# Optimization experiments

Hardware: AMD Instinct MI355X
Metric: run time of the kernel (lower is better)

## Reference

```python
import jax, jax.numpy as jnp
import numpy as np

IN_CAPS, IN_SIZE = 1152, 8
OUT_CAPS, OUT_SIZE = 10, 16
NUM_ITERS = 3


def squash(s, axis=-1, eps=1e-8):
    sq = jnp.sum(s * s, axis=axis, keepdims=True)
    norm = jnp.sqrt(sq + eps)
    return (sq / (1.0 + sq)) * (s / norm)


def setup_inputs() -> dict:
    key = jax.random.key(0)
    kx, kw = jax.random.split(key)
    x = jax.random.normal(kx, (512, IN_CAPS, IN_SIZE), dtype=jnp.float32)
    W = jax.random.normal(kw, (IN_CAPS, OUT_CAPS, OUT_SIZE, IN_SIZE), dtype=jnp.float32)
    return {"x": x, "W": W}


def reference(x, W):
    # u_hat[b,i,o,p] = sum_q W[i,o,p,q] x[b,i,q]   -> [B, I, O, P]
    u_hat = jnp.einsum("iopq,biq->biop", W, x)
    b_ij = jnp.zeros((IN_CAPS, OUT_CAPS), dtype=u_hat.dtype)
    v_j = None
    for _ in range(NUM_ITERS):
        # legacy F.softmax on [1,I,O,1] with no dim -> softmax over dim=1 (in_capsules)
        c_ij = jax.nn.softmax(b_ij, axis=0)                      # [I, O]
        s_j = jnp.einsum("io,biop->bop", c_ij, u_hat)            # [B, O, P]
        v_j = squash(s_j, axis=-1)                               # [B, O, P]
        # agreement, averaged over batch
        u_vj1 = jnp.einsum("biop,bop->io", u_hat, v_j) / x.shape[0]
        b_ij = b_ij + u_vj1
    return v_j  # [B, 10, 16]
```

## Files before the change

### kernel.cpp

```cpp
#include <hip/hip_runtime.h>
#include <hip/hip_bf16.h>

#define B 512
#define IC 1152
#define QD 8
#define OD 10
#define PD 16
#define KD (IC * QD)
#define NKB (KD / 32)
#define NCS 72
#define KSTEPS (NKB / NCS)
#define NCB 4
#define SOP (B * OD * PD)
#define IO (IC * OD)

typedef short bf16x8 __attribute__((ext_vector_type(8)));
typedef float f32x4 __attribute__((ext_vector_type(4)));

__device__ __forceinline__ short f2bf(float f) {
  union { float f; unsigned u; } x;
  x.f = f;
  unsigned r = x.u + 0x7FFFu + ((x.u >> 16) & 1u);
  return (short)(r >> 16);
}

__global__ __launch_bounds__(256) void routebuild_kernel(const float* __restrict__ W,
                                                         const float* __restrict__ u_part,
                                                         float* __restrict__ bijA,
                                                         short* __restrict__ Bs,
                                                         int mode) {
  __shared__ float bl[IO];
  __shared__ float wred[4][OD];
  __shared__ float mx[OD], inv[OD];
  const int tid = threadIdx.x;
  const int wave = tid >> 6, lane = tid & 63;

  if (mode != 0) {
    float lmax[OD];
#pragma unroll
    for (int o = 0; o < OD; ++o) lmax[o] = -1e30f;
    for (int i = tid; i < IC; i += 256) {
      float acc[OD];
      if (mode == 2) {
#pragma unroll
        for (int o = 0; o < OD; ++o) acc[o] = bijA[i * OD + o];
      } else {
#pragma unroll
        for (int o = 0; o < OD; ++o) acc[o] = 0.f;
      }
      for (int bc = 0; bc < NCB; ++bc) {
        const float* up = u_part + (size_t)bc * IO + i * OD;
        const float4 u0 = *(const float4*)up;
        const float4 u1 = *(const float4*)(up + 4);
        const float2 u2 = *(const float2*)(up + 8);
        acc[0] += u0.x; acc[1] += u0.y; acc[2] += u0.z; acc[3] += u0.w;
        acc[4] += u1.x; acc[5] += u1.y; acc[6] += u1.z; acc[7] += u1.w;
        acc[8] += u2.x; acc[9] += u2.y;
      }
#pragma unroll
      for (int o = 0; o < OD; ++o) {
        bl[i * OD + o] = acc[o];
        lmax[o] = fmaxf(lmax[o], acc[o]);
        if (mode == 1 && blockIdx.x == 0) bijA[i * OD + o] = acc[o];
      }
    }
#pragma unroll
    for (int o = 0; o < OD; ++o) {
      float m = lmax[o];
#pragma unroll
      for (int s = 1; s < 64; s <<= 1) m = fmaxf(m, __shfl_xor(m, s));
      if (lane == 0) wred[wave][o] = m;
    }
    __syncthreads();
    if (tid < OD)
      mx[tid] = fmaxf(fmaxf(wred[0][tid], wred[1][tid]),
                      fmaxf(wred[2][tid], wred[3][tid]));
    __syncthreads();
    float lsum[OD];
#pragma unroll
    for (int o = 0; o < OD; ++o) lsum[o] = 0.f;
    for (int i = tid; i < IC; i += 256) {
#pragma unroll
      for (int o = 0; o < OD; ++o) {
        const float e = __expf(bl[i * OD + o] - mx[o]);
        bl[i * OD + o] = e;
        lsum[o] += e;
      }
    }
    __syncthreads();
#pragma unroll
    for (int o = 0; o < OD; ++o) {
      float s = lsum[o];
#pragma unroll
      for (int st = 1; st < 64; st <<= 1) s += __shfl_xor(s, st);
      if (lane == 0) wred[wave][o] = s;
    }
    __syncthreads();
    if (tid < OD)
      inv[tid] = 1.f / (wred[0][tid] + wred[1][tid] + wred[2][tid] + wred[3][tid]);
    __syncthreads();
  }

  const int t = blockIdx.x * 256 + tid;
  const int kb = t / 160, n = t % 160;
  const int o = n >> 4, p = n & 15;
  short ov[32];
#pragma unroll
  for (int quad = 0; quad < 4; ++quad) {
    const int i = kb * 4 + quad;
    const float ci = (mode == 0) ? (1.0f / (float)IC) : (bl[i * OD + o] * inv[o]);
    const float4* wp = (const float4*)(W + (((size_t)i * OD + o) * PD + p) * QD);
    const float4 w0 = wp[0], w1 = wp[1];
    ov[quad * 8 + 0] = f2bf(ci * w0.x); ov[quad * 8 + 1] = f2bf(ci * w0.y);
    ov[quad * 8 + 2] = f2bf(ci * w0.z); ov[quad * 8 + 3] = f2bf(ci * w0.w);
    ov[quad * 8 + 4] = f2bf(ci * w1.x); ov[quad * 8 + 5] = f2bf(ci * w1.y);
    ov[quad * 8 + 6] = f2bf(ci * w1.z); ov[quad * 8 + 7] = f2bf(ci * w1.w);
  }
  int4* dst = (int4*)(Bs + (size_t)t * 32);
  const int4* src = (const int4*)ov;
#pragma unroll
  for (int j = 0; j < 4; ++j) dst[j] = src[j];
}

__global__ __launch_bounds__(256) void sgemm_kernel(const float* __restrict__ x,
                                                    const short* __restrict__ Bs,
                                                    float* __restrict__ s_part) {
  const int tid = threadIdx.x;
  const int wave = tid >> 6, lane = tid & 63;
  const int ln = lane & 15, quad = lane >> 4;
  const int cz = blockIdx.x % NCS, mb = blockIdx.x / NCS;
  const int m0 = mb * 64 + wave * 16;
  f32x4 acc[10] = {};
  const float* arow = x + (size_t)(m0 + ln) * KD + quad * 8;
#pragma unroll
  for (int step = 0; step < KSTEPS; ++step) {
    const int kb = cz * KSTEPS + step;
    const float* ap = arow + kb * 32;
    const f32x4 a0 = *(const f32x4*)ap;
    const f32x4 a1 = *(const f32x4*)(ap + 4);
    bf16x8 af;
    af[0] = f2bf(a0[0]); af[1] = f2bf(a0[1]); af[2] = f2bf(a0[2]); af[3] = f2bf(a0[3]);
    af[4] = f2bf(a1[0]); af[5] = f2bf(a1[1]); af[6] = f2bf(a1[2]); af[7] = f2bf(a1[3]);
    const short* bp = Bs + (size_t)kb * 5120 + ln * 32 + quad * 8;
#pragma unroll
    for (int nt = 0; nt < 10; ++nt) {
      const bf16x8 bf = *(const bf16x8*)(bp + nt * 512);
      acc[nt] = __builtin_amdgcn_mfma_f32_16x16x32_bf16(af, bf, acc[nt], 0, 0, 0);
    }
  }
  float* sp = s_part + (size_t)cz * SOP;
#pragma unroll
  for (int nt = 0; nt < 10; ++nt)
#pragma unroll
    for (int r = 0; r < 4; ++r)
      sp[(size_t)(m0 + quad * 4 + r) * 160 + nt * 16 + ln] = acc[nt][r];
}

__global__ __launch_bounds__(256) void squash_kernel(const float* __restrict__ s_part,
                                                     short* __restrict__ vB,
                                                     float* __restrict__ out,
                                                     int write_out) {
  const int t = blockIdx.x * 256 + threadIdx.x;
  float sv = 0.f;
#pragma unroll 8
  for (int ch = 0; ch < NCS; ++ch) sv += s_part[(size_t)ch * SOP + t];
  float sq = sv * sv;
#pragma unroll
  for (int m = 1; m < 16; m <<= 1) sq += __shfl_xor(sq, m, 16);
  const float norm = sqrtf(sq + 1e-8f);
  const float val = sv * (sq / ((1.f + sq) * norm));
  if (write_out) {
    out[t] = val;
  } else {
    const int b = t / 160, n = t - b * 160;
    vB[((size_t)(b >> 5) * 160 + n) * 32 + (b & 31)] = f2bf(val);
  }
}

__global__ __launch_bounds__(256) void aggemm_kernel(const float* __restrict__ x,
                                                     const float* __restrict__ W,
                                                     const short* __restrict__ vB,
                                                     float* __restrict__ u_part) {
  __shared__ __align__(16) short Abuf[16 * 64 * 8];
  const int tid = threadIdx.x;
  const int ig8 = blockIdx.x, kq = blockIdx.y;
  const int b0 = kq * 128;
#pragma unroll
  for (int j = 0; j < 8; ++j) {
    const int idx = tid + j * 256;
    const int b = idx >> 4, f4 = idx & 15;
    const float4 vx = *(const float4*)(x + (size_t)(b0 + b) * KD + ig8 * 64 + f4 * 4);
    const int kb = b >> 5, qk = (b & 31) >> 3, jj = b & 7;
    const int mt = (f4 * 4) >> 4;
    const int mlb = (f4 & 3) * 4;
    short* dst = Abuf + (((mt * 4 + kb) * 64 + qk * 16 + mlb) * 8 + jj);
    dst[0] = f2bf(vx.x); dst[8] = f2bf(vx.y); dst[16] = f2bf(vx.z); dst[24] = f2bf(vx.w);
  }
  __syncthreads();
  const int mt = tid >> 6, lane = tid & 63;
  const int ln = lane & 15, quad = lane >> 4;
  f32x4 acc[10] = {};
#pragma unroll
  for (int kb = 0; kb < 4; ++kb) {
    const bf16x8 af = *(const bf16x8*)(Abuf + ((mt * 4 + kb) * 64 + lane) * 8);
    const short* bp = vB + ((size_t)(kq * 4 + kb) * 160 + ln) * 32 + quad * 8;
#pragma unroll
    for (int nt = 0; nt < 10; ++nt) {
      const bf16x8 bf = *(const bf16x8*)(bp + nt * 512);
      acc[nt] = __builtin_amdgcn_mfma_f32_16x16x32_bf16(af, bf, acc[nt], 0, 0, 0);
    }
  }
  const int i = ig8 * 8 + mt * 2 + (quad >> 1);
  const int qb = (quad & 1) * 4;
#pragma unroll
  for (int nt = 0; nt < 10; ++nt) {
    const float4 wv = *(const float4*)(W + (((size_t)i * OD + nt) * PD + ln) * QD + qb);
    float pa = acc[nt][0] * wv.x + acc[nt][1] * wv.y + acc[nt][2] * wv.z + acc[nt][3] * wv.w;
    pa += __shfl_xor(pa, 1); pa += __shfl_xor(pa, 2); pa += __shfl_xor(pa, 4);
    pa += __shfl_xor(pa, 8); pa += __shfl_xor(pa, 16);
    if ((lane & 31) == 0)
      u_part[(size_t)kq * IO + i * OD + nt] = pa * (1.0f / (float)B);
  }
}


extern "C" void kernel_launch(void* const* d_in, const int* in_sizes, int n_in,
                              void* d_out, int out_size, void* d_ws, size_t ws_size,
                              hipStream_t stream) {
  const float* x = (const float*)d_in[0];
  const float* W = (const float*)d_in[1];
  float* out = (float*)d_out;

  float* ws = (float*)d_ws;
  float* s_part = ws;
  float* bijA = s_part + (size_t)NCS * SOP;
  float* u_part = bijA + IO;
  short* vB = (short*)(u_part + (size_t)NCB * IO);
  short* Bs = vB + (size_t)16 * 160 * 32;

  const dim3 agrid(144, NCB);

  routebuild_kernel<<<180, 256, 0, stream>>>(W, u_part, bijA, Bs, 0);
  sgemm_kernel<<<8 * NCS, 256, 0, stream>>>(x, Bs, s_part);
  squash_kernel<<<SOP / 256, 256, 0, stream>>>(s_part, vB, out, 0);
  aggemm_kernel<<<agrid, 256, 0, stream>>>(x, W, vB, u_part);
  routebuild_kernel<<<180, 256, 0, stream>>>(W, u_part, bijA, Bs, 1);
  sgemm_kernel<<<8 * NCS, 256, 0, stream>>>(x, Bs, s_part);
  squash_kernel<<<SOP / 256, 256, 0, stream>>>(s_part, vB, out, 0);
  aggemm_kernel<<<agrid, 256, 0, stream>>>(x, W, vB, u_part);
  routebuild_kernel<<<180, 256, 0, stream>>>(W, u_part, bijA, Bs, 2);
  sgemm_kernel<<<8 * NCS, 256, 0, stream>>>(x, Bs, s_part);
  squash_kernel<<<SOP / 256, 256, 0, stream>>>(s_part, vB, out, 1);
}
```

Before: 184.4 us.

## Fuse routing softmax, s-GEMM and squash into one per-output-capsule kernel

Replaces the routebuild/sgemm/squash sequence with one iter_kernel per routing iteration. Each of 80 blocks owns one output capsule and 64 batch rows: it computes that capsule's softmax column and runs the full-K MFMA reduction, scaling W on the fly. It then squashes in registers and writes vB or the output. The agreement kernel now loops over all batch chunks inside one block, so u_t needs no cross-block partial sums and the split-K partial buffers go away. This cuts launches and large partial-sum traffic, but only 80 or 144 blocks run, each doing a long serial K loop, which may leave much of the GPU idle.

```diff
diff --git a/kernel.cpp b/kernel.cpp
--- a/kernel.cpp
+++ b/kernel.cpp
@@ -8,10 +8,6 @@
 #define PD 16
 #define KD (IC * QD)
 #define NKB (KD / 32)
-#define NCS 72
-#define KSTEPS (NKB / NCS)
-#define NCB 4
-#define SOP (B * OD * PD)
 #define IO (IC * OD)
 
 typedef short bf16x8 __attribute__((ext_vector_type(8)));
@@ -23,191 +19,148 @@
   unsigned r = x.u + 0x7FFFu + ((x.u >> 16) & 1u);
   return (short)(r >> 16);
 }
+__device__ __forceinline__ unsigned pkbf(float a, float b) {
+  union { __hip_bfloat162 h; unsigned u; } c;
+  c.h = __float22bfloat162_rn(make_float2(a, b));
+  return c.u;
+}
 
-__global__ __launch_bounds__(256) void routebuild_kernel(const float* __restrict__ W,
-                                                         const float* __restrict__ u_part,
-                                                         float* __restrict__ bijA,
-                                                         short* __restrict__ Bs,
-                                                         int mode) {
-  __shared__ float bl[IO];
-  __shared__ float wred[4][OD];
-  __shared__ float mx[OD], inv[OD];
+__global__ __launch_bounds__(256) void iter_kernel(const float* __restrict__ x,
+                                                   const float* __restrict__ W,
+                                                   const float* __restrict__ u_t,
+                                                   float* __restrict__ bijA,
+                                                   short* __restrict__ vB,
+                                                   float* __restrict__ out,
+                                                   int mode) {
+  __shared__ float cS[IC];
+  __shared__ float redA[4], redB[4];
   const int tid = threadIdx.x;
+  const int mb = blockIdx.x & 7, o = blockIdx.x >> 3;
   const int wave = tid >> 6, lane = tid & 63;
+  const int ln = lane & 15, quad = lane >> 4;
 
+  float inv = 0.f;
   if (mode != 0) {
-    float lmax[OD];
+    float lm = -1e30f;
 #pragma unroll
-    for (int o = 0; o < OD; ++o) lmax[o] = -1e30f;
-    for (int i = tid; i < IC; i += 256) {
-      float acc[OD];
-      if (mode == 2) {
-#pragma unroll
-        for (int o = 0; o < OD; ++o) acc[o] = bijA[i * OD + o];
-      } else {
-#pragma unroll
-        for (int o = 0; o < OD; ++o) acc[o] = 0.f;
-      }
-      for (int bc = 0; bc < NCB; ++bc) {
-        const float* up = u_part + (size_t)bc * IO + i * OD;
-        const float4 u0 = *(const float4*)up;
-        const float4 u1 = *(const float4*)(up + 4);
-        const float2 u2 = *(const float2*)(up + 8);
-        acc[0] += u0.x; acc[1] += u0.y; acc[2] += u0.z; acc[3] += u0.w;
-        acc[4] += u1.x; acc[5] += u1.y; acc[6] += u1.z; acc[7] += u1.w;
-        acc[8] += u2.x; acc[9] += u2.y;
-      }
-#pragma unroll
-      for (int o = 0; o < OD; ++o) {
-        bl[i * OD + o] = acc[o];
-        lmax[o] = fmaxf(lmax[o], acc[o]);
-        if (mode == 1 && blockIdx.x == 0) bijA[i * OD + o] = acc[o];
+    for (int k = 0; k < 5; ++k) {
+      const int i = tid + k * 256;
+      if (i < IC) {
+        float t = u_t[o * IC + i];
+        if (mode == 2) t += bijA[o * IC + i];
+        if (mode == 1 && mb == 0) bijA[o * IC + i] = t;
+        cS[i] = t;
+        lm = fmaxf(lm, t);
       }
     }
 #pragma unroll
-    for (int o = 0; o < OD; ++o) {
-      float m = lmax[o];
+    for (int s = 1; s < 64; s <<= 1) lm = fmaxf(lm, __shfl_xor(lm, s));
+    if (lane == 0) redA[wave] = lm;
+    __syncthreads();
+    const float mx = fmaxf(fmaxf(redA[0], redA[1]), fmaxf(redA[2], redA[3]));
+    float ls = 0.f;
 #pragma unroll
-      for (int s = 1; s < 64; s <<= 1) m = fmaxf(m, __shfl_xor(m, s));
-      if (lane == 0) wred[wave][o] = m;
+    for (int k = 0; k < 5; ++k) {
+      const int i = tid + k * 256;
+      if (i < IC) {
+        const float e = __expf(cS[i] - mx);
+        cS[i] = e;
+        ls += e;
+      }
     }
+#pragma unroll
+    for (int s = 1; s < 64; s <<= 1) ls += __shfl_xor(ls, s);
+    if (lane == 0) redB[wave] = ls;
     __syncthreads();
-    if (tid < OD)
-      mx[tid] = fmaxf(fmaxf(wred[0][tid], wred[1][tid]),
-                      fmaxf(wred[2][tid], wred[3][tid]));
+    inv = 1.f / (redB[0] + redB[1] + redB[2] + redB[3]);
+  }
+
+  const int m0 = mb * 64 + wave * 16;
+  const float* arow = x + (size_t)(m0 + ln) * KD + quad * 8;
+  const float* wrow = W + (o * PD + ln) * QD;
+  const float cu = 1.0f / (float)IC;
+  f32x4 acc0 = {}, acc1 = {};
+#pragma unroll 2
+  for (int kb = 0; kb < NKB; kb += 2) {
+    {
+      const int i = kb * 4 + quad;
+      const float ci = mode ? cS[i] * inv : cu;
+      const f32x4 a0 = *(const f32x4*)(arow + (size_t)kb * 32);
+      const f32x4 a1 = *(const f32x4*)(arow + (size_t)kb * 32 + 4);
+      const f32x4 w0 = *(const f32x4*)(wrow + (size_t)i * 1280);
+      const f32x4 w1 = *(const f32x4*)(wrow + (size_t)i * 1280 + 4);
+      uint4 ap, bp;
+      ap.x = pkbf(a0[0], a0[1]); ap.y = pkbf(a0[2], a0[3]);
+      ap.z = pkbf(a1[0], a1[1]); ap.w = pkbf(a1[2], a1[3]);
+      bp.x = pkbf(ci * w0[0], ci * w0[1]); bp.y = pkbf(ci * w0[2], ci * w0[3]);
+      bp.z = pkbf(ci * w1[0], ci * w1[1]); bp.w = pkbf(ci * w1[2], ci * w1[3]);
+      acc0 = __builtin_amdgcn_mfma_f32_16x16x32_bf16(*(bf16x8*)&ap, *(bf16x8*)&bp, acc0, 0, 0, 0);
+    }
+    {
+      const int i = (kb + 1) * 4 + quad;
+      const float ci = mode ? cS[i] * inv : cu;
+      const f32x4 a0 = *(const f32x4*)(arow + (size_t)(kb + 1) * 32);
+      const f32x4 a1 = *(const f32x4*)(arow + (size_t)(kb + 1) * 32 + 4);
+      const f32x4 w0 = *(const f32x4*)(wrow + (size_t)i * 1280);
+      const f32x4 w1 = *(const f32x4*)(wrow + (size_t)i * 1280 + 4);
+      uint4 ap, bp;
+      ap.x = pkbf(a0[0], a0[1]); ap.y = pkbf(a0[2], a0[3]);
+      ap.z = pkbf(a1[0], a1[1]); ap.w = pkbf(a1[2], a1[3]);
+      bp.x = pkbf(ci * w0[0], ci * w0[1]); bp.y = pkbf(ci * w0[2], ci * w0[3]);
+      bp.z = pkbf(ci * w1[0], ci * w1[1]); bp.w = pkbf(ci * w1[2], ci * w1[3]);
+      acc1 = __builtin_amdgcn_mfma_f32_16x16x32_bf16(*(bf16x8*)&ap, *(bf16x8*)&bp, acc1, 0, 0, 0);
+    }
+  }
+  const f32x4 acc = acc0 + acc1;
+#pragma unroll
+  for (int r = 0; r < 4; ++r) {
+    float sq = acc[r] * acc[r];
+    sq += __shfl_xor(sq, 1); sq += __shfl_xor(sq, 2);
+    sq += __shfl_xor(sq, 4); sq += __shfl_xor(sq, 8);
+    const float norm = sqrtf(sq + 1e-8f);
+    const float val = acc[r] * (sq / ((1.f + sq) * norm));
+    const int b = m0 + quad * 4 + r;
+    if (mode == 2) {
+      out[((size_t)b * OD + o) * PD + ln] = val;
+    } else {
+      vB[((size_t)(b >> 5) * 160 + o * PD + ln) * 32 + (b & 31)] = f2bf(val);
+    }
+  }
+}
+
+__global__ __launch_bounds__(256) void agg_kernel(const float* __restrict__ x,
+                                                  const float* __restrict__ W,
+                                                  const short* __restrict__ vB,
+                                                  float* __restrict__ u_t) {
+  __shared__ __align__(16) short Abuf[16 * 64 * 8];
+  const int tid = threadIdx.x;
+  const int ig8 = blockIdx.x;
+  const int mt = tid >> 6, lane = tid & 63;
+  const int ln = lane & 15, quad = lane >> 4;
+  f32x4 acc[10] = {};
+  for (int kq = 0; kq < 4; ++kq) {
+    const int b0 = kq * 128;
     __syncthreads();
-    float lsum[OD];
 #pragma unroll
-    for (int o = 0; o < OD; ++o) lsum[o] = 0.f;
-    for (int i = tid; i < IC; i += 256) {
-#pragma unroll
-      for (int o = 0; o < OD; ++o) {
-        const float e = __expf(bl[i * OD + o] - mx[o]);
-        bl[i * OD + o] = e;
-        lsum[o] += e;
-      }
+    for (int j = 0; j < 8; ++j) {
+      const int idx = tid + j * 256;
+      const int b = idx >> 4, f4 = idx & 15;
+      const float4 vx = *(const float4*)(x + (size_t)(b0 + b) * KD + ig8 * 64 + f4 * 4);
+      const int kbl = b >> 5, qk = (b & 31) >> 3, jj = b & 7;
+      const int mtt = f4 >> 2, mlb = (f4 & 3) * 4;
+      short* dst = Abuf + (((mtt * 4 + kbl) * 64 + qk * 16 + mlb) * 8 + jj);
+      dst[0] = f2bf(vx.x); dst[8] = f2bf(vx.y); dst[16] = f2bf(vx.z); dst[24] = f2bf(vx.w);
     }
     __syncthreads();
 #pragma unroll
-    for (int o = 0; o < OD; ++o) {
-      float s = lsum[o];
+    for (int kbb = 0; kbb < 4; ++kbb) {
+      const bf16x8 af = *(const bf16x8*)(Abuf + ((mt * 4 + kbb) * 64 + lane) * 8);
+      const short* bp = vB + ((size_t)((kq * 4 + kbb) * 160) + ln) * 32 + quad * 8;
 #pragma unroll
-      for (int st = 1; st < 64; st <<= 1) s += __shfl_xor(s, st);
-      if (lane == 0) wred[wave][o] = s;
-    }
-    __syncthreads();
-    if (tid < OD)
-      inv[tid] = 1.f / (wred[0][tid] + wred[1][tid] + wred[2][tid] + wred[3][tid]);
-    __syncthreads();
-  }
-
-  const int t = blockIdx.x * 256 + tid;
-  const int kb = t / 160, n = t % 160;
-  const int o = n >> 4, p = n & 15;
-  short ov[32];
-#pragma unroll
-  for (int quad = 0; quad < 4; ++quad) {
-    const int i = kb * 4 + quad;
-    const float ci = (mode == 0) ? (1.0f / (float)IC) : (bl[i * OD + o] * inv[o]);
-    const float4* wp = (const float4*)(W + (((size_t)i * OD + o) * PD + p) * QD);
-    const float4 w0 = wp[0], w1 = wp[1];
-    ov[quad * 8 + 0] = f2bf(ci * w0.x); ov[quad * 8 + 1] = f2bf(ci * w0.y);
-    ov[quad * 8 + 2] = f2bf(ci * w0.z); ov[quad * 8 + 3] = f2bf(ci * w0.w);
-    ov[quad * 8 + 4] = f2bf(ci * w1.x); ov[quad * 8 + 5] = f2bf(ci * w1.y);
-    ov[quad * 8 + 6] = f2bf(ci * w1.z); ov[quad * 8 + 7] = f2bf(ci * w1.w);
-  }
-  int4* dst = (int4*)(Bs + (size_t)t * 32);
-  const int4* src = (const int4*)ov;
-#pragma unroll
-  for (int j = 0; j < 4; ++j) dst[j] = src[j];
-}
-
-__global__ __launch_bounds__(256) void sgemm_kernel(const float* __restrict__ x,
-                                                    const short* __restrict__ Bs,
-                                                    float* __restrict__ s_part) {
-  const int tid = threadIdx.x;
-  const int wave = tid >> 6, lane = tid & 63;
-  const int ln = lane & 15, quad = lane >> 4;
-  const int cz = blockIdx.x % NCS, mb = blockIdx.x / NCS;
-  const int m0 = mb * 64 + wave * 16;
-  f32x4 acc[10] = {};
-  const float* arow = x + (size_t)(m0 + ln) * KD + quad * 8;
-#pragma unroll
-  for (int step = 0; step < KSTEPS; ++step) {
-    const int kb = cz * KSTEPS + step;
-    const float* ap = arow + kb * 32;
-    const f32x4 a0 = *(const f32x4*)ap;
-    const f32x4 a1 = *(const f32x4*)(ap + 4);
-    bf16x8 af;
-    af[0] = f2bf(a0[0]); af[1] = f2bf(a0[1]); af[2] = f2bf(a0[2]); af[3] = f2bf(a0[3]);
-    af[4] = f2bf(a1[0]); af[5] = f2bf(a1[1]); af[6] = f2bf(a1[2]); af[7] = f2bf(a1[3]);
-    const short* bp = Bs + (size_t)kb * 5120 + ln * 32 + quad * 8;
-#pragma unroll
-    for (int nt = 0; nt < 10; ++nt) {
-      const bf16x8 bf = *(const bf16x8*)(bp + nt * 512);
-      acc[nt] = __builtin_amdgcn_mfma_f32_16x16x32_bf16(af, bf, acc[nt], 0, 0, 0);
-    }
-  }
-  float* sp = s_part + (size_t)cz * SOP;
-#pragma unroll
-  for (int nt = 0; nt < 10; ++nt)
-#pragma unroll
-    for (int r = 0; r < 4; ++r)
-      sp[(size_t)(m0 + quad * 4 + r) * 160 + nt * 16 + ln] = acc[nt][r];
-}
-
-__global__ __launch_bounds__(256) void squash_kernel(const float* __restrict__ s_part,
-                                                     short* __restrict__ vB,
-                                                     float* __restrict__ out,
-                                                     int write_out) {
-  const int t = blockIdx.x * 256 + threadIdx.x;
-  float sv = 0.f;
-#pragma unroll 8
-  for (int ch = 0; ch < NCS; ++ch) sv += s_part[(size_t)ch * SOP + t];
-  float sq = sv * sv;
-#pragma unroll
-  for (int m = 1; m < 16; m <<= 1) sq += __shfl_xor(sq, m, 16);
-  const float norm = sqrtf(sq + 1e-8f);
-  const float val = sv * (sq / ((1.f + sq) * norm));
-  if (write_out) {
-    out[t] = val;
-  } else {
-    const int b = t / 160, n = t - b * 160;
-    vB[((size_t)(b >> 5) * 160 + n) * 32 + (b & 31)] = f2bf(val);
-  }
-}
-
-__global__ __launch_bounds__(256) void aggemm_kernel(const float* __restrict__ x,
-                                                     const float* __restrict__ W,
-                                                     const short* __restrict__ vB,
-                                                     float* __restrict__ u_part) {
-  __shared__ __align__(16) short Abuf[16 * 64 * 8];
-  const int tid = threadIdx.x;
-  const int ig8 = blockIdx.x, kq = blockIdx.y;
-  const int b0 = kq * 128;
-#pragma unroll
-  for (int j = 0; j < 8; ++j) {
-    const int idx = tid + j * 256;
-    const int b = idx >> 4, f4 = idx & 15;
-    const float4 vx = *(const float4*)(x + (size_t)(b0 + b) * KD + ig8 * 64 + f4 * 4);
-    const int kb = b >> 5, qk = (b & 31) >> 3, jj = b & 7;
-    const int mt = (f4 * 4) >> 4;
-    const int mlb = (f4 & 3) * 4;
-    short* dst = Abuf + (((mt * 4 + kb) * 64 + qk * 16 + mlb) * 8 + jj);
-    dst[0] = f2bf(vx.x); dst[8] = f2bf(vx.y); dst[16] = f2bf(vx.z); dst[24] = f2bf(vx.w);
-  }
-  __syncthreads();
-  const int mt = tid >> 6, lane = tid & 63;
-  const int ln = lane & 15, quad = lane >> 4;
-  f32x4 acc[10] = {};
-#pragma unroll
-  for (int kb = 0; kb < 4; ++kb) {
-    const bf16x8 af = *(const bf16x8*)(Abuf + ((mt * 4 + kb) * 64 + lane) * 8);
-    const short* bp = vB + ((size_t)(kq * 4 + kb) * 160 + ln) * 32 + quad * 8;
-#pragma unroll
-    for (int nt = 0; nt < 10; ++nt) {
-      const bf16x8 bf = *(const bf16x8*)(bp + nt * 512);
-      acc[nt] = __builtin_amdgcn_mfma_f32_16x16x32_bf16(af, bf, acc[nt], 0, 0, 0);
+      for (int nt = 0; nt < 10; ++nt) {
+        const bf16x8 bf = *(const bf16x8*)(bp + nt * 512);
+        acc[nt] = __builtin_amdgcn_mfma_f32_16x16x32_bf16(af, bf, acc[nt], 0, 0, 0);
+      }
     }
   }
   const int i = ig8 * 8 + mt * 2 + (quad >> 1);
@@ -218,8 +171,7 @@
     float pa = acc[nt][0] * wv.x + acc[nt][1] * wv.y + acc[nt][2] * wv.z + acc[nt][3] * wv.w;
     pa += __shfl_xor(pa, 1); pa += __shfl_xor(pa, 2); pa += __shfl_xor(pa, 4);
     pa += __shfl_xor(pa, 8); pa += __shfl_xor(pa, 16);
-    if ((lane & 31) == 0)
-      u_part[(size_t)kq * IO + i * OD + nt] = pa * (1.0f / (float)B);
+    if ((lane & 31) == 0) u_t[(size_t)nt * IC + i] = pa * (1.0f / (float)B);
   }
 }
 
@@ -232,23 +184,13 @@
   float* out = (float*)d_out;
 
   float* ws = (float*)d_ws;
-  float* s_part = ws;
-  float* bijA = s_part + (size_t)NCS * SOP;
-  float* u_part = bijA + IO;
-  short* vB = (short*)(u_part + (size_t)NCB * IO);
-  short* Bs = vB + (size_t)16 * 160 * 32;
+  float* u_t = ws;
+  float* bijA = u_t + IO;
+  short* vB = (short*)(bijA + IO);
 
-  const dim3 agrid(144, NCB);
-
-  routebuild_kernel<<<180, 256, 0, stream>>>(W, u_part, bijA, Bs, 0);
-  sgemm_kernel<<<8 * NCS, 256, 0, stream>>>(x, Bs, s_part);
-  squash_kernel<<<SOP / 256, 256, 0, stream>>>(s_part, vB, out, 0);
-  aggemm_kernel<<<agrid, 256, 0, stream>>>(x, W, vB, u_part);
-  routebuild_kernel<<<180, 256, 0, stream>>>(W, u_part, bijA, Bs, 1);
-  sgemm_kernel<<<8 * NCS, 256, 0, stream>>>(x, Bs, s_part);
-  squash_kernel<<<SOP / 256, 256, 0, stream>>>(s_part, vB, out, 0);
-  aggemm_kernel<<<agrid, 256, 0, stream>>>(x, W, vB, u_part);
-  routebuild_kernel<<<180, 256, 0, stream>>>(W, u_part, bijA, Bs, 2);
-  sgemm_kernel<<<8 * NCS, 256, 0, stream>>>(x, Bs, s_part);
-  squash_kernel<<<SOP / 256, 256, 0, stream>>>(s_part, vB, out, 1);
+  iter_kernel<<<80, 256, 0, stream>>>(x, W, u_t, bijA, vB, out, 0);
+  agg_kernel<<<144, 256, 0, stream>>>(x, W, vB, u_t);
+  iter_kernel<<<80, 256, 0, stream>>>(x, W, u_t, bijA, vB, out, 1);
+  agg_kernel<<<144, 256, 0, stream>>>(x, W, vB, u_t);
+  iter_kernel<<<80, 256, 0, stream>>>(x, W, u_t, bijA, vB, out, 2);
 }
```

Result: slower. 524.1 us (+184.3%).

## Fuse dependent stages into paired kernels synchronized by global atomic counters

Applied to the files above, without the earlier changes.

Merges each sgemm+squash pair and each agreement-GEMM+route-build pair into single launches. Consumer blocks spin on a device-scope atomic counter until all producer blocks finish, which cuts the number of kernel launches and the gaps between them. The agreement GEMM now loops over the four batch chunks inside each block, so the four-way u_part partial reduction is gone, and u is written transposed. The spin-wait depends on all producer blocks being resident or scheduled ahead of the waiting blocks, which risks deadlock or idle CUs while consumers spin.

```diff
diff --git a/kernel.cpp b/kernel.cpp
--- a/kernel.cpp
+++ b/kernel.cpp
@@ -10,9 +10,11 @@
 #define NKB (KD / 32)
 #define NCS 72
 #define KSTEPS (NKB / NCS)
-#define NCB 4
+#define SUNITS 576
+#define AUNITS 144
+#define RBBLK 180
+#define IO (IC * OD)
 #define SOP (B * OD * PD)
-#define IO (IC * OD)
 
 typedef short bf16x8 __attribute__((ext_vector_type(8)));
 typedef float f32x4 __attribute__((ext_vector_type(4)));
@@ -24,44 +26,177 @@
   return (short)(r >> 16);
 }
 
-__global__ __launch_bounds__(256) void routebuild_kernel(const float* __restrict__ W,
-                                                         const float* __restrict__ u_part,
-                                                         float* __restrict__ bijA,
-                                                         short* __restrict__ Bs,
-                                                         int mode) {
-  __shared__ float bl[IO];
-  __shared__ float wred[4][OD];
-  __shared__ float mx[OD], inv[OD];
+__device__ __forceinline__ void signal_done(int* cnt) {
+  __syncthreads();
+  if (threadIdx.x == 0) {
+    __threadfence();
+    __hip_atomic_fetch_add(cnt, 1, __ATOMIC_RELEASE, __HIP_MEMORY_SCOPE_AGENT);
+  }
+}
+__device__ __forceinline__ void wait_done(int* cnt, int target) {
+  if (threadIdx.x == 0) {
+    while (__hip_atomic_load(cnt, __ATOMIC_RELAXED, __HIP_MEMORY_SCOPE_AGENT) < target)
+      __builtin_amdgcn_s_sleep(8);
+    __threadfence();
+  }
+  __syncthreads();
+}
+
+__global__ __launch_bounds__(256) void rb0_kernel(const float* __restrict__ W,
+                                                  short* __restrict__ Bs,
+                                                  int* __restrict__ cnt) {
+  if (blockIdx.x == 0 && threadIdx.x < 8) cnt[threadIdx.x] = 0;
+  const int t = blockIdx.x * 256 + threadIdx.x;
+  const int kb = t / 160, n = t % 160;
+  const int o = n >> 4, p = n & 15;
+  const float cu = 1.0f / (float)IC;
+  short ov[32];
+#pragma unroll
+  for (int quad = 0; quad < 4; ++quad) {
+    const int i = kb * 4 + quad;
+    const float4* wp = (const float4*)(W + (((size_t)i * OD + o) * PD + p) * QD);
+    const float4 w0 = wp[0], w1 = wp[1];
+    ov[quad * 8 + 0] = f2bf(cu * w0.x); ov[quad * 8 + 1] = f2bf(cu * w0.y);
+    ov[quad * 8 + 2] = f2bf(cu * w0.z); ov[quad * 8 + 3] = f2bf(cu * w0.w);
+    ov[quad * 8 + 4] = f2bf(cu * w1.x); ov[quad * 8 + 5] = f2bf(cu * w1.y);
+    ov[quad * 8 + 6] = f2bf(cu * w1.z); ov[quad * 8 + 7] = f2bf(cu * w1.w);
+  }
+  int4* dst = (int4*)(Bs + (size_t)t * 32);
+  const int4* src = (const int4*)ov;
+#pragma unroll
+  for (int j = 0; j < 4; ++j) dst[j] = src[j];
+}
+
+__global__ __launch_bounds__(256) void d1_kernel(const float* __restrict__ x,
+                                                 const short* __restrict__ Bs,
+                                                 float* __restrict__ s_part,
+                                                 short* __restrict__ vB,
+                                                 float* __restrict__ out,
+                                                 int* __restrict__ cnt,
+                                                 int write_out) {
   const int tid = threadIdx.x;
-  const int wave = tid >> 6, lane = tid & 63;
-
-  if (mode != 0) {
+  if (blockIdx.x < SUNITS) {
+    const int wave = tid >> 6, lane = tid & 63;
+    const int ln = lane & 15, quad = lane >> 4;
+    const int cz = blockIdx.x % NCS, mb = blockIdx.x / NCS;
+    const int m0 = mb * 64 + wave * 16;
+    f32x4 acc[10] = {};
+    const float* arow = x + (size_t)(m0 + ln) * KD + quad * 8;
+#pragma unroll
+    for (int step = 0; step < KSTEPS; ++step) {
+      const int kb = cz * KSTEPS + step;
+      const float* ap = arow + (size_t)kb * 32;
+      const f32x4 a0 = *(const f32x4*)ap;
+      const f32x4 a1 = *(const f32x4*)(ap + 4);
+      bf16x8 af;
+      af[0] = f2bf(a0[0]); af[1] = f2bf(a0[1]); af[2] = f2bf(a0[2]); af[3] = f2bf(a0[3]);
+      af[4] = f2bf(a1[0]); af[5] = f2bf(a1[1]); af[6] = f2bf(a1[2]); af[7] = f2bf(a1[3]);
+      const short* bp = Bs + (size_t)kb * 5120 + ln * 32 + quad * 8;
+#pragma unroll
+      for (int nt = 0; nt < 10; ++nt) {
+        const bf16x8 bf = *(const bf16x8*)(bp + nt * 512);
+        acc[nt] = __builtin_amdgcn_mfma_f32_16x16x32_bf16(af, bf, acc[nt], 0, 0, 0);
+      }
+    }
+    float* sp = s_part + (size_t)cz * SOP;
+#pragma unroll
+    for (int nt = 0; nt < 10; ++nt)
+#pragma unroll
+      for (int r = 0; r < 4; ++r)
+        sp[(size_t)(m0 + quad * 4 + r) * 160 + nt * 16 + ln] = acc[nt][r];
+    signal_done(cnt);
+  } else {
+    wait_done(cnt, SUNITS);
+    const int t = (blockIdx.x - SUNITS) * 256 + tid;
+    float sv = 0.f;
+#pragma unroll 8
+    for (int ch = 0; ch < NCS; ++ch) sv += s_part[(size_t)ch * SOP + t];
+    float sq = sv * sv;
+#pragma unroll
+    for (int m = 1; m < 16; m <<= 1) sq += __shfl_xor(sq, m, 16);
+    const float norm = sqrtf(sq + 1e-8f);
+    const float val = sv * (sq / ((1.f + sq) * norm));
+    if (write_out) {
+      out[t] = val;
+    } else {
+      const int b = t / 160, n = t - b * 160;
+      vB[((size_t)(b >> 5) * 160 + n) * 32 + (b & 31)] = f2bf(val);
+    }
+  }
+}
+
+__global__ __launch_bounds__(256) void d2_kernel(const float* __restrict__ x,
+                                                 const float* __restrict__ W,
+                                                 const short* __restrict__ vB,
+                                                 float* __restrict__ u_t,
+                                                 float* __restrict__ bijA,
+                                                 short* __restrict__ Bs,
+                                                 int* __restrict__ cnt,
+                                                 int mode) {
+  __shared__ __align__(16) char smem[48000];
+  const int tid = threadIdx.x;
+  if (blockIdx.x < AUNITS) {
+    short* Abuf = (short*)smem;
+    const int ig8 = blockIdx.x;
+    const int mt = tid >> 6, lane = tid & 63;
+    const int ln = lane & 15, quad = lane >> 4;
+    f32x4 acc[10] = {};
+    for (int kq = 0; kq < 4; ++kq) {
+      const int b0 = kq * 128;
+      __syncthreads();
+#pragma unroll
+      for (int j = 0; j < 8; ++j) {
+        const int idx = tid + j * 256;
+        const int b = idx >> 4, f4 = idx & 15;
+        const float4 vx = *(const float4*)(x + (size_t)(b0 + b) * KD + ig8 * 64 + f4 * 4);
+        const int kbl = b >> 5, qk = (b & 31) >> 3, jj = b & 7;
+        const int mtt = f4 >> 2, mlb = (f4 & 3) * 4;
+        short* dst = Abuf + (((mtt * 4 + kbl) * 64 + qk * 16 + mlb) * 8 + jj);
+        dst[0] = f2bf(vx.x); dst[8] = f2bf(vx.y); dst[16] = f2bf(vx.z); dst[24] = f2bf(vx.w);
+      }
+      __syncthreads();
+#pragma unroll
+      for (int kbb = 0; kbb < 4; ++kbb) {
+        const bf16x8 af = *(const bf16x8*)(Abuf + ((mt * 4 + kbb) * 64 + lane) * 8);
+        const short* bp = vB + ((size_t)((kq * 4 + kbb) * 160) + ln) * 32 + quad * 8;
+#pragma unroll
+        for (int nt = 0; nt < 10; ++nt) {
+          const bf16x8 bf = *(const bf16x8*)(bp + nt * 512);
+          acc[nt] = __builtin_amdgcn_mfma_f32_16x16x32_bf16(af, bf, acc[nt], 0, 0, 0);
+        }
+      }
+    }
+    const int lane2 = tid & 63;
+    const int ln2 = lane2 & 15, quad2 = lane2 >> 4;
+    const int i = ig8 * 8 + (tid >> 6) * 2 + (quad2 >> 1);
+    const int qb = (quad2 & 1) * 4;
+#pragma unroll
+    for (int nt = 0; nt < 10; ++nt) {
+      const float4 wv = *(const float4*)(W + (((size_t)i * OD + nt) * PD + ln2) * QD + qb);
+      float pa = acc[nt][0] * wv.x + acc[nt][1] * wv.y + acc[nt][2] * wv.z + acc[nt][3] * wv.w;
+      pa += __shfl_xor(pa, 1); pa += __shfl_xor(pa, 2); pa += __shfl_xor(pa, 4);
+      pa += __shfl_xor(pa, 8); pa += __shfl_xor(pa, 16);
+      if ((lane2 & 31) == 0) u_t[(size_t)nt * IC + i] = pa * (1.0f / (float)B);
+    }
+    signal_done(cnt);
+  } else {
+    float* bl = (float*)smem;
+    __shared__ float wred[4][OD];
+    __shared__ float mxS[OD], invS[OD];
+    const int tb = blockIdx.x - AUNITS;
+    const int wave = tid >> 6, lane = tid & 63;
+    wait_done(cnt, AUNITS);
     float lmax[OD];
 #pragma unroll
     for (int o = 0; o < OD; ++o) lmax[o] = -1e30f;
     for (int i = tid; i < IC; i += 256) {
-      float acc[OD];
-      if (mode == 2) {
-#pragma unroll
-        for (int o = 0; o < OD; ++o) acc[o] = bijA[i * OD + o];
-      } else {
-#pragma unroll
-        for (int o = 0; o < OD; ++o) acc[o] = 0.f;
-      }
-      for (int bc = 0; bc < NCB; ++bc) {
-        const float* up = u_part + (size_t)bc * IO + i * OD;
-        const float4 u0 = *(const float4*)up;
-        const float4 u1 = *(const float4*)(up + 4);
-        const float2 u2 = *(const float2*)(up + 8);
-        acc[0] += u0.x; acc[1] += u0.y; acc[2] += u0.z; acc[3] += u0.w;
-        acc[4] += u1.x; acc[5] += u1.y; acc[6] += u1.z; acc[7] += u1.w;
-        acc[8] += u2.x; acc[9] += u2.y;
-      }
 #pragma unroll
       for (int o = 0; o < OD; ++o) {
-        bl[i * OD + o] = acc[o];
-        lmax[o] = fmaxf(lmax[o], acc[o]);
-        if (mode == 1 && blockIdx.x == 0) bijA[i * OD + o] = acc[o];
+        float t = u_t[o * IC + i];
+        if (mode == 2) t += bijA[o * IC + i];
+        if (mode == 1 && tb == 0) bijA[o * IC + i] = t;
+        bl[i * OD + o] = t;
+        lmax[o] = fmaxf(lmax[o], t);
       }
     }
 #pragma unroll
@@ -73,8 +208,8 @@
     }
     __syncthreads();
     if (tid < OD)
-      mx[tid] = fmaxf(fmaxf(wred[0][tid], wred[1][tid]),
-                      fmaxf(wred[2][tid], wred[3][tid]));
+      mxS[tid] = fmaxf(fmaxf(wred[0][tid], wred[1][tid]),
+                       fmaxf(wred[2][tid], wred[3][tid]));
     __syncthreads();
     float lsum[OD];
 #pragma unroll
@@ -82,7 +217,7 @@
     for (int i = tid; i < IC; i += 256) {
 #pragma unroll
       for (int o = 0; o < OD; ++o) {
-        const float e = __expf(bl[i * OD + o] - mx[o]);
+        const float e = __expf(bl[i * OD + o] - mxS[o]);
         bl[i * OD + o] = e;
         lsum[o] += e;
       }
@@ -97,129 +232,27 @@
     }
     __syncthreads();
     if (tid < OD)
-      inv[tid] = 1.f / (wred[0][tid] + wred[1][tid] + wred[2][tid] + wred[3][tid]);
-    __syncthreads();
-  }
-
-  const int t = blockIdx.x * 256 + tid;
-  const int kb = t / 160, n = t % 160;
-  const int o = n >> 4, p = n & 15;
-  short ov[32];
-#pragma unroll
-  for (int quad = 0; quad < 4; ++quad) {
-    const int i = kb * 4 + quad;
-    const float ci = (mode == 0) ? (1.0f / (float)IC) : (bl[i * OD + o] * inv[o]);
-    const float4* wp = (const float4*)(W + (((size_t)i * OD + o) * PD + p) * QD);
-    const float4 w0 = wp[0], w1 = wp[1];
-    ov[quad * 8 + 0] = f2bf(ci * w0.x); ov[quad * 8 + 1] = f2bf(ci * w0.y);
-    ov[quad * 8 + 2] = f2bf(ci * w0.z); ov[quad * 8 + 3] = f2bf(ci * w0.w);
-    ov[quad * 8 + 4] = f2bf(ci * w1.x); ov[quad * 8 + 5] = f2bf(ci * w1.y);
-    ov[quad * 8 + 6] = f2bf(ci * w1.z); ov[quad * 8 + 7] = f2bf(ci * w1.w);
-  }
-  int4* dst = (int4*)(Bs + (size_t)t * 32);
-  const int4* src = (const int4*)ov;
-#pragma unroll
-  for (int j = 0; j < 4; ++j) dst[j] = src[j];
-}
-
-__global__ __launch_bounds__(256) void sgemm_kernel(const float* __restrict__ x,
-                                                    const short* __restrict__ Bs,
-                                                    float* __restrict__ s_part) {
-  const int tid = threadIdx.x;
-  const int wave = tid >> 6, lane = tid & 63;
-  const int ln = lane & 15, quad = lane >> 4;
-  const int cz = blockIdx.x % NCS, mb = blockIdx.x / NCS;
-  const int m0 = mb * 64 + wave * 16;
-  f32x4 acc[10] = {};
-  const float* arow = x + (size_t)(m0 + ln) * KD + quad * 8;
-#pragma unroll
-  for (int step = 0; step < KSTEPS; ++step) {
-    const int kb = cz * KSTEPS + step;
-    const float* ap = arow + kb * 32;
-    const f32x4 a0 = *(const f32x4*)ap;
-    const f32x4 a1 = *(const f32x4*)(ap + 4);
-    bf16x8 af;
-    af[0] = f2bf(a0[0]); af[1] = f2bf(a0[1]); af[2] = f2bf(a0[2]); af[3] = f2bf(a0[3]);
-    af[4] = f2bf(a1[0]); af[5] = f2bf(a1[1]); af[6] = f2bf(a1[2]); af[7] = f2bf(a1[3]);
-    const short* bp = Bs + (size_t)kb * 5120 + ln * 32 + quad * 8;
-#pragma unroll
-    for (int nt = 0; nt < 10; ++nt) {
-      const bf16x8 bf = *(const bf16x8*)(bp + nt * 512);
-      acc[nt] = __builtin_amdgcn_mfma_f32_16x16x32_bf16(af, bf, acc[nt], 0, 0, 0);
-    }
-  }
-  float* sp = s_part + (size_t)cz * SOP;
-#pragma unroll
-  for (int nt = 0; nt < 10; ++nt)
-#pragma unroll
-    for (int r = 0; r < 4; ++r)
-      sp[(size_t)(m0 + quad * 4 + r) * 160 + nt * 16 + ln] = acc[nt][r];
-}
-
-__global__ __launch_bounds__(256) void squash_kernel(const float* __restrict__ s_part,
-                                                     short* __restrict__ vB,
-                                                     float* __restrict__ out,
-                                                     int write_out) {
-  const int t = blockIdx.x * 256 + threadIdx.x;
-  float sv = 0.f;
-#pragma unroll 8
-  for (int ch = 0; ch < NCS; ++ch) sv += s_part[(size_t)ch * SOP + t];
-  float sq = sv * sv;
-#pragma unroll
-  for (int m = 1; m < 16; m <<= 1) sq += __shfl_xor(sq, m, 16);
-  const float norm = sqrtf(sq + 1e-8f);
-  const float val = sv * (sq / ((1.f + sq) * norm));
-  if (write_out) {
-    out[t] = val;
-  } else {
-    const int b = t / 160, n = t - b * 160;
-    vB[((size_t)(b >> 5) * 160 + n) * 32 + (b & 31)] = f2bf(val);
-  }
-}
-
-__global__ __launch_bounds__(256) void aggemm_kernel(const float* __restrict__ x,
-                                                     const float* __restrict__ W,
-                                                     const short* __restrict__ vB,
-                                                     float* __restrict__ u_part) {
-  __shared__ __align__(16) short Abuf[16 * 64 * 8];
-  const int tid = threadIdx.x;
-  const int ig8 = blockIdx.x, kq = blockIdx.y;
-  const int b0 = kq * 128;
-#pragma unroll
-  for (int j = 0; j < 8; ++j) {
-    const int idx = tid + j * 256;
-    const int b = idx >> 4, f4 = idx & 15;
-    const float4 vx = *(const float4*)(x + (size_t)(b0 + b) * KD + ig8 * 64 + f4 * 4);
-    const int kb = b >> 5, qk = (b & 31) >> 3, jj = b & 7;
-    const int mt = (f4 * 4) >> 4;
-    const int mlb = (f4 & 3) * 4;
-    short* dst = Abuf + (((mt * 4 + kb) * 64 + qk * 16 + mlb) * 8 + jj);
-    dst[0] = f2bf(vx.x); dst[8] = f2bf(vx.y); dst[16] = f2bf(vx.z); dst[24] = f2bf(vx.w);
-  }
-  __syncthreads();
-  const int mt = tid >> 6, lane = tid & 63;
-  const int ln = lane & 15, quad = lane >> 4;
-  f32x4 acc[10] = {};
-#pragma unroll
-  for (int kb = 0; kb < 4; ++kb) {
-    const bf16x8 af = *(const bf16x8*)(Abuf + ((mt * 4 + kb) * 64 + lane) * 8);
-    const short* bp = vB + ((size_t)(kq * 4 + kb) * 160 + ln) * 32 + quad * 8;
-#pragma unroll
-    for (int nt = 0; nt < 10; ++nt) {
-      const bf16x8 bf = *(const bf16x8*)(bp + nt * 512);
-      acc[nt] = __builtin_amdgcn_mfma_f32_16x16x32_bf16(af, bf, acc[nt], 0, 0, 0);
-    }
-  }
-  const int i = ig8 * 8 + mt * 2 + (quad >> 1);
-  const int qb = (quad & 1) * 4;
-#pragma unroll
-  for (int nt = 0; nt < 10; ++nt) {
-    const float4 wv = *(const float4*)(W + (((size_t)i * OD + nt) * PD + ln) * QD + qb);
-    float pa = acc[nt][0] * wv.x + acc[nt][1] * wv.y + acc[nt][2] * wv.z + acc[nt][3] * wv.w;
-    pa += __shfl_xor(pa, 1); pa += __shfl_xor(pa, 2); pa += __shfl_xor(pa, 4);
-    pa += __shfl_xor(pa, 8); pa += __shfl_xor(pa, 16);
-    if ((lane & 31) == 0)
-      u_part[(size_t)kq * IO + i * OD + nt] = pa * (1.0f / (float)B);
+      invS[tid] = 1.f / (wred[0][tid] + wred[1][tid] + wred[2][tid] + wred[3][tid]);
+    __syncthreads();
+    const int t = tb * 256 + tid;
+    const int kb = t / 160, n = t % 160;
+    const int o = n >> 4, p = n & 15;
+    short ov[32];
+#pragma unroll
+    for (int quad = 0; quad < 4; ++quad) {
+      const int i = kb * 4 + quad;
+      const float ci = bl[i * OD + o] * invS[o];
+      const float4* wp = (const float4*)(W + (((size_t)i * OD + o) * PD + p) * QD);
+      const float4 w0 = wp[0], w1 = wp[1];
+      ov[quad * 8 + 0] = f2bf(ci * w0.x); ov[quad * 8 + 1] = f2bf(ci * w0.y);
+      ov[quad * 8 + 2] = f2bf(ci * w0.z); ov[quad * 8 + 3] = f2bf(ci * w0.w);
+      ov[quad * 8 + 4] = f2bf(ci * w1.x); ov[quad * 8 + 5] = f2bf(ci * w1.y);
+      ov[quad * 8 + 6] = f2bf(ci * w1.z); ov[quad * 8 + 7] = f2bf(ci * w1.w);
+    }
+    int4* dst = (int4*)(Bs + (size_t)t * 32);
+    const int4* src = (const int4*)ov;
+#pragma unroll
+    for (int j = 0; j < 4; ++j) dst[j] = src[j];
   }
 }
 
@@ -233,22 +266,16 @@
 
   float* ws = (float*)d_ws;
   float* s_part = ws;
-  float* bijA = s_part + (size_t)NCS * SOP;
-  float* u_part = bijA + IO;
-  short* vB = (short*)(u_part + (size_t)NCB * IO);
+  float* u_t = s_part + (size_t)NCS * SOP;
+  float* bijA = u_t + IO;
+  short* vB = (short*)(bijA + IO);
   short* Bs = vB + (size_t)16 * 160 * 32;
-
-  const dim3 agrid(144, NCB);
-
-  routebuild_kernel<<<180, 256, 0, stream>>>(W, u_part, bijA, Bs, 0);
-  sgemm_kernel<<<8 * NCS, 256, 0, stream>>>(x, Bs, s_part);
-  squash_kernel<<<SOP / 256, 256, 0, stream>>>(s_part, vB, out, 0);
-  aggemm_kernel<<<agrid, 256, 0, stream>>>(x, W, vB, u_part);
-  routebuild_kernel<<<180, 256, 0, stream>>>(W, u_part, bijA, Bs, 1);
-  sgemm_kernel<<<8 * NCS, 256, 0, stream>>>(x, Bs, s_part);
-  squash_kernel<<<SOP / 256, 256, 0, stream>>>(s_part, vB, out, 0);
-  aggemm_kernel<<<agrid, 256, 0, stream>>>(x, W, vB, u_part);
-  routebuild_kernel<<<180, 256, 0, stream>>>(W, u_part, bijA, Bs, 2);
-  sgemm_kernel<<<8 * NCS, 256, 0, stream>>>(x, Bs, s_part);
-  squash_kernel<<<SOP / 256, 256, 0, stream>>>(s_part, vB, out, 1);
-}
+  int* cnt = (int*)(Bs + (size_t)NKB * 160 * 32);
+
+  rb0_kernel<<<RBBLK, 256, 0, stream>>>(W, Bs, cnt);
+  d1_kernel<<<SUNITS + 320, 256, 0, stream>>>(x, Bs, s_part, vB, out, cnt + 0, 0);
+  d2_kernel<<<AUNITS + RBBLK, 256, 0, stream>>>(x, W, vB, u_t, bijA, Bs, cnt + 1, 1);
+  d1_kernel<<<SUNITS + 320, 256, 0, stream>>>(x, Bs, s_part, vB, out, cnt + 2, 0);
+  d2_kernel<<<AUNITS + RBBLK, 256, 0, stream>>>(x, W, vB, u_t, bijA, Bs, cnt + 3, 2);
+  d1_kernel<<<SUNITS + 320, 256, 0, stream>>>(x, Bs, s_part, vB, out, cnt + 4, 1);
+}
```

Result: slower. 521.9 us (+183.1%).
